# Performance work log

Measured on AMD Instinct MI355X. Metric: run time of the kernel, lower is better.

The kernel has to match this reference:

```python
import jax, jax.numpy as jnp
import numpy as np

SEQ, BZ, DIM = 2048, 16, 1024
NUM_LANG, DICT_LEN = 16, 32000


def setup_inputs() -> dict:
    key = jax.random.key(0)
    ks = jax.random.split(key, 6)
    x = jax.random.normal(ks[0], (SEQ, BZ, DIM), dtype=jnp.float32)
    # raw language ids live at the tail of the dictionary: dict_len-1-raw in [0, num_lang)
    raw = DICT_LEN - 1 - jax.random.randint(ks[1], (BZ,), 0, NUM_LANG)
    W_base = jax.random.normal(ks[2], (DIM, DIM), dtype=jnp.float32) * (DIM ** -0.5)
    b_base = jax.random.normal(ks[3], (DIM,), dtype=jnp.float32) * 0.02
    W = jax.random.uniform(ks[4], (NUM_LANG, DIM, DIM), dtype=jnp.float32) * (DIM ** -0.5)
    bias = jax.random.uniform(ks[5], (NUM_LANG, DIM), dtype=jnp.float32)
    return {"x": x, "lang_ids": raw, "W_base": W_base, "b_base": b_base,
            "W": W, "bias": bias, "dict_len": DICT_LEN, "num_lang": NUM_LANG}


def reference(x, lang_ids, W_base, b_base, W, bias, dict_len, num_lang):
    # Map raw ids to expert indices in [0, num_lang)
    ids = dict_len - 1 - lang_ids                      # [bz]
    # base_model (nn.Linear): h = x @ W_base.T + b_base
    h = jnp.einsum('sbd,ed->sbe', x, W_base) + b_base  # [seq, bz, dim]
    # The original pads each language group to max group size, runs a batched
    # einsum 'abcd,ade->abce' over languages, then scatters back with per-lang
    # bias. Mathematically each batch column j gets W[lang_j] applied:
    We = W[ids]                                        # [bz, dim, dim]
    out = jnp.einsum('sbd,bde->sbe', h, We) + bias[ids][None, :, :]
    return out
```

## Files before the change

kernel.cpp:

```cpp
#include <hip/hip_runtime.h>
#include <stdint.h>

typedef unsigned short u16;
typedef unsigned int u32;
typedef __bf16 bf16x8 __attribute__((ext_vector_type(8)));
typedef float f32x4 __attribute__((ext_vector_type(4)));

#define SEQ 2048
#define BZ 16
#define DIM 1024

__device__ __forceinline__ u16 f2bf(float f) {
    union { float f; u32 u; } a; a.f = f;
    u32 r = a.u + 0x7FFFu + ((a.u >> 16) & 1u);
    return (u16)(r >> 16);
}
__device__ __forceinline__ float bf2f(u16 u) {
    union { u32 u; float f; } a; a.u = ((u32)u) << 16;
    return a.f;
}
__device__ __forceinline__ void async16(const u16* g, u16* l) {
    __builtin_amdgcn_global_load_lds(
        (const __attribute__((address_space(1))) void*)g,
        (__attribute__((address_space(3))) void*)l, 16, 0, 0);
}

__global__ void convert_x(const float* __restrict__ x, u16* __restrict__ xb)
{
    int s = blockIdx.x;
    int t = threadIdx.x;
    const float4* src = (const float4*)(x + (size_t)s * BZ * DIM);
    #pragma unroll
    for (int j = 0; j < 16; j++) {
        int idx = j * 256 + t;
        float4 v = src[idx];
        int e = idx * 4;
        int b = e >> 10, d = e & 1023;
        u32 lo = f2bf(v.x) | ((u32)f2bf(v.y) << 16);
        u32 hi = f2bf(v.z) | ((u32)f2bf(v.w) << 16);
        *(uint2*)(xb + ((size_t)b * SEQ + s) * DIM + d) = make_uint2(lo, hi);
    }
}

__global__ void transpose_cvt(const float* __restrict__ W,
                              const float* __restrict__ W_base,
                              const int* __restrict__ lang_ids,
                              const int* __restrict__ dict_len,
                              u16* __restrict__ Wt,
                              u16* __restrict__ Wbt)
{
    int z = blockIdx.z;
    const float* S;
    u16* D;
    if (z < BZ) {
        int id = dict_len[0] - 1 - lang_ids[z];
        S = W + (size_t)id * DIM * DIM;
        D = Wbt + (size_t)z * DIM * DIM;
    } else {
        S = W_base;
        D = Wt;
    }
    __shared__ float tile[32][33];
    int tx = threadIdx.x, ty = threadIdx.y;
    int x0 = blockIdx.x * 32, y0 = blockIdx.y * 32;
    #pragma unroll
    for (int i = 0; i < 4; i++)
        tile[ty + 8 * i][tx] = S[(size_t)(y0 + ty + 8 * i) * DIM + x0 + tx];
    __syncthreads();
    #pragma unroll
    for (int i = 0; i < 4; i++)
        D[(size_t)(x0 + ty + 8 * i) * DIM + y0 + tx] = f2bf(tile[tx][ty + 8 * i]);
}

__global__ void bb_kernel(const u16* __restrict__ Wbt,
                          const float* __restrict__ b_base,
                          const float* __restrict__ bias,
                          const int* __restrict__ lang_ids,
                          const int* __restrict__ dict_len,
                          float* __restrict__ bb)
{
    int gw = blockIdx.x * 4 + (threadIdx.x >> 6);
    int b = gw >> 10;
    int f = gw & 1023;
    int lane = threadIdx.x & 63;
    const u16* row = Wbt + ((size_t)b * DIM + f) * DIM;
    float s = 0.f;
    #pragma unroll
    for (int i = 0; i < DIM / 64; i++)
        s += bf2f(row[lane + 64 * i]) * b_base[lane + 64 * i];
    #pragma unroll
    for (int off = 32; off; off >>= 1)
        s += __shfl_xor(s, off, 64);
    if (lane == 0) {
        int id = dict_len[0] - 1 - lang_ids[b];
        bb[b * DIM + f] = s + bias[(size_t)id * DIM + f];
    }
}

__global__ void gemm1_kernel(const u16* __restrict__ Wbt,
                             const u16* __restrict__ Wt,
                             u16* __restrict__ CT)
{
    int bid = blockIdx.x;
    int virt = ((bid & 7) << 7) + (bid >> 3);
    int b    = virt >> 6;
    int rem  = virt & 63;
    int f0   = (rem >> 3) << 7;
    int d0   = (rem & 7) << 7;

    const u16* A = Wbt + (size_t)b * DIM * DIM;
    const u16* B = Wt;
    u16* C = CT + (size_t)b * DIM * DIM;

    __shared__ u16 As[2 * 128 * 32];
    __shared__ u16 Bs[2 * 128 * 32];

    int tid = threadIdx.x;
    int wave = tid >> 6, lane = tid & 63;
    int wm = (wave >> 1) * 64, wn = (wave & 1) * 64;
    int quad = lane >> 4, lr = lane & 15;

    int srow = wave * 32 + (lane >> 2);
    int scol = (lane & 3) * 8;
    const u16* ga0 = A + (size_t)(f0 + srow) * DIM + scol;
    const u16* ga1 = ga0 + (size_t)16 * DIM;
    const u16* gb0 = B + (size_t)(d0 + srow) * DIM + scol;
    const u16* gb1 = gb0 + (size_t)16 * DIM;
    int lofs = wave * 32 * 32;

    f32x4 acc[4][4];
    #pragma unroll
    for (int i = 0; i < 4; i++)
        #pragma unroll
        for (int j = 0; j < 4; j++)
            #pragma unroll
            for (int e = 0; e < 4; e++) acc[i][j][e] = 0.f;

    async16(ga0, As + lofs); async16(ga1, As + lofs + 16 * 32);
    async16(gb0, Bs + lofs); async16(gb1, Bs + lofs + 16 * 32);
    ga0 += 32; ga1 += 32; gb0 += 32; gb1 += 32;
    __syncthreads();

    int cur = 0;
    for (int k0 = 0; k0 < DIM; k0 += 32) {
        int nxt = cur ^ 1;
        if (k0 + 32 < DIM) {
            u16* da = As + nxt * 4096 + lofs;
            u16* db = Bs + nxt * 4096 + lofs;
            async16(ga0, da); async16(ga1, da + 16 * 32);
            async16(gb0, db); async16(gb1, db + 16 * 32);
            ga0 += 32; ga1 += 32; gb0 += 32; gb1 += 32;
        }
        const u16* ra = As + cur * 4096;
        const u16* rb = Bs + cur * 4096;
        bf16x8 af[4], bfv[4];
        #pragma unroll
        for (int mt = 0; mt < 4; mt++)
            af[mt] = *(const bf16x8*)&ra[(wm + mt * 16 + lr) * 32 + quad * 8];
        #pragma unroll
        for (int nt = 0; nt < 4; nt++)
            bfv[nt] = *(const bf16x8*)&rb[(wn + nt * 16 + lr) * 32 + quad * 8];
        #pragma unroll
        for (int mt = 0; mt < 4; mt++)
            #pragma unroll
            for (int nt = 0; nt < 4; nt++)
                acc[mt][nt] = __builtin_amdgcn_mfma_f32_16x16x32_bf16(
                    af[mt], bfv[nt], acc[mt][nt], 0, 0, 0);
        __syncthreads();
        cur = nxt;
    }
    #pragma unroll
    for (int mt = 0; mt < 4; mt++) {
        int fr = f0 + wm + mt * 16 + quad * 4;
        #pragma unroll
        for (int nt = 0; nt < 4; nt++) {
            int dc = d0 + wn + nt * 16 + lr;
            #pragma unroll
            for (int rr = 0; rr < 4; rr++)
                C[(size_t)(fr + rr) * DIM + dc] = f2bf(acc[mt][nt][rr]);
        }
    }
}

__global__ void gemm2_kernel(const u16* __restrict__ xb,
                             const u16* __restrict__ CT,
                             const float* __restrict__ bb,
                             float* __restrict__ out)
{
    int bid = blockIdx.x;
    int virt = ((bid & 7) << 8) + (bid >> 3);
    int b    = virt >> 7;
    int rem  = virt & 127;
    int s0   = (rem >> 3) << 7;
    int f0   = (rem & 7) << 7;

    const u16* A  = xb + (size_t)b * SEQ * DIM;
    const u16* Bm = CT + (size_t)b * DIM * DIM;

    __shared__ u16 As[2 * 128 * 32];
    __shared__ u16 Bs[2 * 128 * 32];

    int tid = threadIdx.x;
    int wave = tid >> 6, lane = tid & 63;
    int wm = (wave >> 1) * 64, wn = (wave & 1) * 64;
    int quad = lane >> 4, lr = lane & 15;

    int srow = wave * 32 + (lane >> 2);
    int scol = (lane & 3) * 8;
    const u16* ga0 = A + (size_t)(s0 + srow) * DIM + scol;
    const u16* ga1 = ga0 + (size_t)16 * DIM;
    const u16* gb0 = Bm + (size_t)(f0 + srow) * DIM + scol;
    const u16* gb1 = gb0 + (size_t)16 * DIM;
    int lofs = wave * 32 * 32;

    f32x4 acc[4][4];
    #pragma unroll
    for (int i = 0; i < 4; i++)
        #pragma unroll
        for (int j = 0; j < 4; j++)
            #pragma unroll
            for (int e = 0; e < 4; e++) acc[i][j][e] = 0.f;

    async16(ga0, As + lofs); async16(ga1, As + lofs + 16 * 32);
    async16(gb0, Bs + lofs); async16(gb1, Bs + lofs + 16 * 32);
    ga0 += 32; ga1 += 32; gb0 += 32; gb1 += 32;
    __syncthreads();

    int cur = 0;
    for (int k0 = 0; k0 < DIM; k0 += 32) {
        int nxt = cur ^ 1;
        if (k0 + 32 < DIM) {
            u16* da = As + nxt * 4096 + lofs;
            u16* db = Bs + nxt * 4096 + lofs;
            async16(ga0, da); async16(ga1, da + 16 * 32);
            async16(gb0, db); async16(gb1, db + 16 * 32);
            ga0 += 32; ga1 += 32; gb0 += 32; gb1 += 32;
        }
        const u16* ra = As + cur * 4096;
        const u16* rb = Bs + cur * 4096;
        bf16x8 af[4], bfv[4];
        #pragma unroll
        for (int mt = 0; mt < 4; mt++)
            af[mt] = *(const bf16x8*)&ra[(wm + mt * 16 + lr) * 32 + quad * 8];
        #pragma unroll
        for (int nt = 0; nt < 4; nt++)
            bfv[nt] = *(const bf16x8*)&rb[(wn + nt * 16 + lr) * 32 + quad * 8];
        #pragma unroll
        for (int mt = 0; mt < 4; mt++)
            #pragma unroll
            for (int nt = 0; nt < 4; nt++)
                acc[mt][nt] = __builtin_amdgcn_mfma_f32_16x16x32_bf16(
                    af[mt], bfv[nt], acc[mt][nt], 0, 0, 0);
        __syncthreads();
        cur = nxt;
    }
    #pragma unroll
    for (int nt = 0; nt < 4; nt++) {
        int fcol = f0 + wn + nt * 16 + lr;
        float bv = bb[b * DIM + fcol];
        #pragma unroll
        for (int mt = 0; mt < 4; mt++) {
            int sr = s0 + wm + mt * 16 + quad * 4;
            #pragma unroll
            for (int rr = 0; rr < 4; rr++)
                out[((size_t)(sr + rr) * BZ + b) * DIM + fcol] = acc[mt][nt][rr] + bv;
        }
    }
}

extern "C" void kernel_launch(void* const* d_in, const int* in_sizes, int n_in,
                              void* d_out, int out_size, void* d_ws, size_t ws_size,
                              hipStream_t stream)
{
    const float* x        = (const float*)d_in[0];
    const int*   lang_ids = (const int*)d_in[1];
    const float* W_base   = (const float*)d_in[2];
    const float* b_base   = (const float*)d_in[3];
    const float* W        = (const float*)d_in[4];
    const float* bias     = (const float*)d_in[5];
    const int*   dict_len = (const int*)d_in[6];
    float* out = (float*)d_out;

    char* ws = (char*)d_ws;
    u16*  Wt  = (u16*)ws;
    u16*  Wbt = (u16*)(ws + (size_t)(2u << 20));
    u16*  CT  = (u16*)(ws + (size_t)(34u << 20));
    float* bb = (float*)(ws + (size_t)(66u << 20));
    u16*  xb  = (u16*)(ws + (size_t)(67u << 20));

    convert_x<<<dim3(SEQ, 1, 1), 256, 0, stream>>>(x, xb);
    transpose_cvt<<<dim3(32, 32, 17), dim3(32, 8, 1), 0, stream>>>(
        W, W_base, lang_ids, dict_len, Wt, Wbt);
    bb_kernel<<<dim3(4096, 1, 1), 256, 0, stream>>>(
        Wbt, b_base, bias, lang_ids, dict_len, bb);
    gemm1_kernel<<<dim3(1024, 1, 1), 256, 0, stream>>>(Wbt, Wt, CT);
    gemm2_kernel<<<dim3(2048, 1, 1), 256, 0, stream>>>(xb, CT, bb, out);
}
```

Before: 425.6 us.

## Use 128x256 tiles with 32x32x16 MFMA and XOR-swizzled LDS in both GEMMs

Both GEMM kernels move from 128x128 block tiles built on 16x16x32 MFMAs to 128x256 tiles built on 32x32x16 MFMAs. Each wave now owns a 128x64 output strip, which raises arithmetic intensity per LDS read and halves the number of blocks. The LDS layout is XOR-swizzled on 16-byte chunks to cut bank conflicts on fragment reads, and launch bounds request two blocks per CU. In exchange it uses more accumulator registers and LDS per block, which may lower occupancy, and the output stores become more strided.

```diff
diff --git a/kernel.cpp b/kernel.cpp
--- a/kernel.cpp
+++ b/kernel.cpp
@@ -5,6 +5,7 @@
 typedef unsigned int u32;
 typedef __bf16 bf16x8 __attribute__((ext_vector_type(8)));
 typedef float f32x4 __attribute__((ext_vector_type(4)));
+typedef float f32x16 __attribute__((ext_vector_type(16)));
 
 #define SEQ 2048
 #define BZ 16
@@ -97,174 +98,218 @@
     }
 }
 
-__global__ void gemm1_kernel(const u16* __restrict__ Wbt,
-                             const u16* __restrict__ Wt,
-                             u16* __restrict__ CT)
+
+#define RD_A(m, kk, l) (((m)*32 + ((l) & 31)) * 32 + ((((kk)*2 + ((l) >> 5)) ^ ((l) & 3)) * 8))
+#define RD_B(w, n, kk, l) (((w)*64 + (n)*32 + ((l) & 31)) * 32 + ((((kk)*2 + ((l) >> 5)) ^ ((l) & 3)) * 8))
+
+__global__ __launch_bounds__(256, 2)
+void gemm1_kernel(const u16* __restrict__ Wbt,
+                  const u16* __restrict__ Wt,
+                  u16* __restrict__ CT)
+{
+    int bid = blockIdx.x;
+    int virt = ((bid & 7) << 6) + (bid >> 3);
+    int b    = virt >> 5;
+    int rem  = virt & 31;
+    int m0   = (rem >> 2) << 7;
+    int n0   = (rem & 3) << 8;
+
+    const u16* A = Wbt + (size_t)b * DIM * DIM;
+    const u16* B = Wt;
+    u16* C = CT + (size_t)b * DIM * DIM;
+
+    __shared__ u16 As[2 * 128 * 32];
+    __shared__ u16 Bs[2 * 256 * 32];
+
+    int tid = threadIdx.x;
+    int w = tid >> 6, l = tid & 63;
+    int lr = l & 31, h = l >> 5;
+
+    int srow = l >> 2;
+    int chunk = (l & 3) ^ (srow & 3);
+    const u16* gA[2]; const u16* gB[4];
+    int lA[2], lB[4];
+    #pragma unroll
+    for (int j = 0; j < 2; j++) {
+        int row = w * 32 + j * 16 + srow;
+        gA[j] = A + (size_t)(m0 + row) * DIM + chunk * 8;
+        lA[j] = (w * 32 + j * 16) * 32;
+    }
+    #pragma unroll
+    for (int j = 0; j < 4; j++) {
+        int row = w * 64 + j * 16 + srow;
+        gB[j] = B + (size_t)(n0 + row) * DIM + chunk * 8;
+        lB[j] = (w * 64 + j * 16) * 32;
+    }
+
+    f32x16 acc[4][2];
+    #pragma unroll
+    for (int m = 0; m < 4; m++)
+        #pragma unroll
+        for (int n = 0; n < 2; n++)
+            #pragma unroll
+            for (int e = 0; e < 16; e++) acc[m][n][e] = 0.f;
+
+    #pragma unroll
+    for (int j = 0; j < 2; j++) async16(gA[j], As + lA[j]);
+    #pragma unroll
+    for (int j = 0; j < 4; j++) async16(gB[j], Bs + lB[j]);
+    #pragma unroll
+    for (int j = 0; j < 2; j++) gA[j] += 32;
+    #pragma unroll
+    for (int j = 0; j < 4; j++) gB[j] += 32;
+    __syncthreads();
+
+    int cur = 0;
+    for (int t = 0; t < DIM / 32; t++) {
+        if (t + 1 < DIM / 32) {
+            int ao = (cur ^ 1) * 4096, bo = (cur ^ 1) * 8192;
+            #pragma unroll
+            for (int j = 0; j < 2; j++) { async16(gA[j], As + ao + lA[j]); gA[j] += 32; }
+            #pragma unroll
+            for (int j = 0; j < 4; j++) { async16(gB[j], Bs + bo + lB[j]); gB[j] += 32; }
+        }
+        const u16* ra = As + cur * 4096;
+        const u16* rb = Bs + cur * 8192;
+        bf16x8 af[4][2], bfv[2][2];
+        #pragma unroll
+        for (int m = 0; m < 4; m++)
+            #pragma unroll
+            for (int kk = 0; kk < 2; kk++)
+                af[m][kk] = *(const bf16x8*)&ra[RD_A(m, kk, l)];
+        #pragma unroll
+        for (int n = 0; n < 2; n++)
+            #pragma unroll
+            for (int kk = 0; kk < 2; kk++)
+                bfv[n][kk] = *(const bf16x8*)&rb[RD_B(w, n, kk, l)];
+        #pragma unroll
+        for (int kk = 0; kk < 2; kk++)
+            #pragma unroll
+            for (int m = 0; m < 4; m++)
+                #pragma unroll
+                for (int n = 0; n < 2; n++)
+                    acc[m][n] = __builtin_amdgcn_mfma_f32_32x32x16_bf16(
+                        af[m][kk], bfv[n][kk], acc[m][n], 0, 0, 0);
+        __syncthreads();
+        cur ^= 1;
+    }
+
+    #pragma unroll
+    for (int m = 0; m < 4; m++)
+        #pragma unroll
+        for (int n = 0; n < 2; n++) {
+            int col = n0 + w * 64 + n * 32 + lr;
+            #pragma unroll
+            for (int reg = 0; reg < 16; reg++) {
+                int row = m0 + m * 32 + (reg & 3) + 8 * (reg >> 2) + 4 * h;
+                C[(size_t)row * DIM + col] = f2bf(acc[m][n][reg]);
+            }
+        }
+}
+
+__global__ __launch_bounds__(256, 2)
+void gemm2_kernel(const u16* __restrict__ xb,
+                  const u16* __restrict__ CT,
+                  const float* __restrict__ bb,
+                  float* __restrict__ out)
 {
     int bid = blockIdx.x;
     int virt = ((bid & 7) << 7) + (bid >> 3);
     int b    = virt >> 6;
     int rem  = virt & 63;
-    int f0   = (rem >> 3) << 7;
-    int d0   = (rem & 7) << 7;
-
-    const u16* A = Wbt + (size_t)b * DIM * DIM;
-    const u16* B = Wt;
-    u16* C = CT + (size_t)b * DIM * DIM;
+    int s0   = (rem >> 2) << 7;
+    int f0   = (rem & 3) << 8;
+
+    const u16* A  = xb + (size_t)b * SEQ * DIM;
+    const u16* Bm = CT + (size_t)b * DIM * DIM;
 
     __shared__ u16 As[2 * 128 * 32];
-    __shared__ u16 Bs[2 * 128 * 32];
+    __shared__ u16 Bs[2 * 256 * 32];
 
     int tid = threadIdx.x;
-    int wave = tid >> 6, lane = tid & 63;
-    int wm = (wave >> 1) * 64, wn = (wave & 1) * 64;
-    int quad = lane >> 4, lr = lane & 15;
-
-    int srow = wave * 32 + (lane >> 2);
-    int scol = (lane & 3) * 8;
-    const u16* ga0 = A + (size_t)(f0 + srow) * DIM + scol;
-    const u16* ga1 = ga0 + (size_t)16 * DIM;
-    const u16* gb0 = B + (size_t)(d0 + srow) * DIM + scol;
-    const u16* gb1 = gb0 + (size_t)16 * DIM;
-    int lofs = wave * 32 * 32;
-
-    f32x4 acc[4][4];
-    #pragma unroll
-    for (int i = 0; i < 4; i++)
-        #pragma unroll
-        for (int j = 0; j < 4; j++)
-            #pragma unroll
-            for (int e = 0; e < 4; e++) acc[i][j][e] = 0.f;
-
-    async16(ga0, As + lofs); async16(ga1, As + lofs + 16 * 32);
-    async16(gb0, Bs + lofs); async16(gb1, Bs + lofs + 16 * 32);
-    ga0 += 32; ga1 += 32; gb0 += 32; gb1 += 32;
+    int w = tid >> 6, l = tid & 63;
+    int lr = l & 31, h = l >> 5;
+
+    int srow = l >> 2;
+    int chunk = (l & 3) ^ (srow & 3);
+    const u16* gA[2]; const u16* gB[4];
+    int lA[2], lB[4];
+    #pragma unroll
+    for (int j = 0; j < 2; j++) {
+        int row = w * 32 + j * 16 + srow;
+        gA[j] = A + (size_t)(s0 + row) * DIM + chunk * 8;
+        lA[j] = (w * 32 + j * 16) * 32;
+    }
+    #pragma unroll
+    for (int j = 0; j < 4; j++) {
+        int row = w * 64 + j * 16 + srow;
+        gB[j] = Bm + (size_t)(f0 + row) * DIM + chunk * 8;
+        lB[j] = (w * 64 + j * 16) * 32;
+    }
+
+    f32x16 acc[4][2];
+    #pragma unroll
+    for (int m = 0; m < 4; m++)
+        #pragma unroll
+        for (int n = 0; n < 2; n++)
+            #pragma unroll
+            for (int e = 0; e < 16; e++) acc[m][n][e] = 0.f;
+
+    #pragma unroll
+    for (int j = 0; j < 2; j++) async16(gA[j], As + lA[j]);
+    #pragma unroll
+    for (int j = 0; j < 4; j++) async16(gB[j], Bs + lB[j]);
+    #pragma unroll
+    for (int j = 0; j < 2; j++) gA[j] += 32;
+    #pragma unroll
+    for (int j = 0; j < 4; j++) gB[j] += 32;
     __syncthreads();
 
     int cur = 0;
-    for (int k0 = 0; k0 < DIM; k0 += 32) {
-        int nxt = cur ^ 1;
-        if (k0 + 32 < DIM) {
-            u16* da = As + nxt * 4096 + lofs;
-            u16* db = Bs + nxt * 4096 + lofs;
-            async16(ga0, da); async16(ga1, da + 16 * 32);
-            async16(gb0, db); async16(gb1, db + 16 * 32);
-            ga0 += 32; ga1 += 32; gb0 += 32; gb1 += 32;
+    for (int t = 0; t < DIM / 32; t++) {
+        if (t + 1 < DIM / 32) {
+            int ao = (cur ^ 1) * 4096, bo = (cur ^ 1) * 8192;
+            #pragma unroll
+            for (int j = 0; j < 2; j++) { async16(gA[j], As + ao + lA[j]); gA[j] += 32; }
+            #pragma unroll
+            for (int j = 0; j < 4; j++) { async16(gB[j], Bs + bo + lB[j]); gB[j] += 32; }
         }
         const u16* ra = As + cur * 4096;
-        const u16* rb = Bs + cur * 4096;
-        bf16x8 af[4], bfv[4];
-        #pragma unroll
-        for (int mt = 0; mt < 4; mt++)
-            af[mt] = *(const bf16x8*)&ra[(wm + mt * 16 + lr) * 32 + quad * 8];
-        #pragma unroll
-        for (int nt = 0; nt < 4; nt++)
-            bfv[nt] = *(const bf16x8*)&rb[(wn + nt * 16 + lr) * 32 + quad * 8];
-        #pragma unroll
-        for (int mt = 0; mt < 4; mt++)
-            #pragma unroll
-            for (int nt = 0; nt < 4; nt++)
-                acc[mt][nt] = __builtin_amdgcn_mfma_f32_16x16x32_bf16(
-                    af[mt], bfv[nt], acc[mt][nt], 0, 0, 0);
+        const u16* rb = Bs + cur * 8192;
+        bf16x8 af[4][2], bfv[2][2];
+        #pragma unroll
+        for (int m = 0; m < 4; m++)
+            #pragma unroll
+            for (int kk = 0; kk < 2; kk++)
+                af[m][kk] = *(const bf16x8*)&ra[RD_A(m, kk, l)];
+        #pragma unroll
+        for (int n = 0; n < 2; n++)
+            #pragma unroll
+            for (int kk = 0; kk < 2; kk++)
+                bfv[n][kk] = *(const bf16x8*)&rb[RD_B(w, n, kk, l)];
+        #pragma unroll
+        for (int kk = 0; kk < 2; kk++)
+            #pragma unroll
+            for (int m = 0; m < 4; m++)
+                #pragma unroll
+                for (int n = 0; n < 2; n++)
+                    acc[m][n] = __builtin_amdgcn_mfma_f32_32x32x16_bf16(
+                        af[m][kk], bfv[n][kk], acc[m][n], 0, 0, 0);
         __syncthreads();
-        cur = nxt;
-    }
-    #pragma unroll
-    for (int mt = 0; mt < 4; mt++) {
-        int fr = f0 + wm + mt * 16 + quad * 4;
-        #pragma unroll
-        for (int nt = 0; nt < 4; nt++) {
-            int dc = d0 + wn + nt * 16 + lr;
-            #pragma unroll
-            for (int rr = 0; rr < 4; rr++)
-                C[(size_t)(fr + rr) * DIM + dc] = f2bf(acc[mt][nt][rr]);
-        }
-    }
-}
-
-__global__ void gemm2_kernel(const u16* __restrict__ xb,
-                             const u16* __restrict__ CT,
-                             const float* __restrict__ bb,
-                             float* __restrict__ out)
-{
-    int bid = blockIdx.x;
-    int virt = ((bid & 7) << 8) + (bid >> 3);
-    int b    = virt >> 7;
-    int rem  = virt & 127;
-    int s0   = (rem >> 3) << 7;
-    int f0   = (rem & 7) << 7;
-
-    const u16* A  = xb + (size_t)b * SEQ * DIM;
-    const u16* Bm = CT + (size_t)b * DIM * DIM;
-
-    __shared__ u16 As[2 * 128 * 32];
-    __shared__ u16 Bs[2 * 128 * 32];
-
-    int tid = threadIdx.x;
-    int wave = tid >> 6, lane = tid & 63;
-    int wm = (wave >> 1) * 64, wn = (wave & 1) * 64;
-    int quad = lane >> 4, lr = lane & 15;
-
-    int srow = wave * 32 + (lane >> 2);
-    int scol = (lane & 3) * 8;
-    const u16* ga0 = A + (size_t)(s0 + srow) * DIM + scol;
-    const u16* ga1 = ga0 + (size_t)16 * DIM;
-    const u16* gb0 = Bm + (size_t)(f0 + srow) * DIM + scol;
-    const u16* gb1 = gb0 + (size_t)16 * DIM;
-    int lofs = wave * 32 * 32;
-
-    f32x4 acc[4][4];
-    #pragma unroll
-    for (int i = 0; i < 4; i++)
-        #pragma unroll
-        for (int j = 0; j < 4; j++)
-            #pragma unroll
-            for (int e = 0; e < 4; e++) acc[i][j][e] = 0.f;
-
-    async16(ga0, As + lofs); async16(ga1, As + lofs + 16 * 32);
-    async16(gb0, Bs + lofs); async16(gb1, Bs + lofs + 16 * 32);
-    ga0 += 32; ga1 += 32; gb0 += 32; gb1 += 32;
-    __syncthreads();
-
-    int cur = 0;
-    for (int k0 = 0; k0 < DIM; k0 += 32) {
-        int nxt = cur ^ 1;
-        if (k0 + 32 < DIM) {
-            u16* da = As + nxt * 4096 + lofs;
-            u16* db = Bs + nxt * 4096 + lofs;
-            async16(ga0, da); async16(ga1, da + 16 * 32);
-            async16(gb0, db); async16(gb1, db + 16 * 32);
-            ga0 += 32; ga1 += 32; gb0 += 32; gb1 += 32;
-        }
-        const u16* ra = As + cur * 4096;
-        const u16* rb = Bs + cur * 4096;
-        bf16x8 af[4], bfv[4];
-        #pragma unroll
-        for (int mt = 0; mt < 4; mt++)
-            af[mt] = *(const bf16x8*)&ra[(wm + mt * 16 + lr) * 32 + quad * 8];
-        #pragma unroll
-        for (int nt = 0; nt < 4; nt++)
-            bfv[nt] = *(const bf16x8*)&rb[(wn + nt * 16 + lr) * 32 + quad * 8];
-        #pragma unroll
-        for (int mt = 0; mt < 4; mt++)
-            #pragma unroll
-            for (int nt = 0; nt < 4; nt++)
-                acc[mt][nt] = __builtin_amdgcn_mfma_f32_16x16x32_bf16(
-                    af[mt], bfv[nt], acc[mt][nt], 0, 0, 0);
-        __syncthreads();
-        cur = nxt;
-    }
-    #pragma unroll
-    for (int nt = 0; nt < 4; nt++) {
-        int fcol = f0 + wn + nt * 16 + lr;
-        float bv = bb[b * DIM + fcol];
-        #pragma unroll
-        for (int mt = 0; mt < 4; mt++) {
-            int sr = s0 + wm + mt * 16 + quad * 4;
-            #pragma unroll
-            for (int rr = 0; rr < 4; rr++)
-                out[((size_t)(sr + rr) * BZ + b) * DIM + fcol] = acc[mt][nt][rr] + bv;
-        }
+        cur ^= 1;
+    }
+
+    #pragma unroll
+    for (int n = 0; n < 2; n++) {
+        int col = f0 + w * 64 + n * 32 + lr;
+        float bv = bb[b * DIM + col];
+        #pragma unroll
+        for (int m = 0; m < 4; m++)
+            #pragma unroll
+            for (int reg = 0; reg < 16; reg++) {
+                int row = s0 + m * 32 + (reg & 3) + 8 * (reg >> 2) + 4 * h;
+                out[((size_t)row * BZ + b) * DIM + col] = acc[m][n][reg] + bv;
+            }
     }
 }
 
@@ -293,6 +338,6 @@
         W, W_base, lang_ids, dict_len, Wt, Wbt);
     bb_kernel<<<dim3(4096, 1, 1), 256, 0, stream>>>(
         Wbt, b_base, bias, lang_ids, dict_len, bb);
-    gemm1_kernel<<<dim3(1024, 1, 1), 256, 0, stream>>>(Wbt, Wt, CT);
-    gemm2_kernel<<<dim3(2048, 1, 1), 256, 0, stream>>>(xb, CT, bb, out);
-}
+    gemm1_kernel<<<dim3(512, 1, 1), 256, 0, stream>>>(Wbt, Wt, CT);
+    gemm2_kernel<<<dim3(1024, 1, 1), 256, 0, stream>>>(xb, CT, bb, out);
+}
```

Result: slower. 441.7 us (+3.8%).
